# Performance work log

Measured on AMD Instinct MI355X. Metric: run time of the kernel, lower is better.

## Reference

```python
import jax, jax.numpy as jnp
import numpy as np

LENGTH = 512
Q = 2 * LENGTH + 3  # num_states = 2*length + 3
ALPHA = 26          # amino-acid alphabet size
BATCH = 256
T = 512


def setup_inputs() -> dict:
    key = jax.random.key(0)
    k1, k2, k3, k4 = jax.random.split(key, 4)
    x = jax.random.randint(k1, (BATCH, T), 0, ALPHA, dtype=jnp.int32)
    A_logits = jax.random.normal(k2, (Q, Q), dtype=jnp.float32)
    B_logits = jax.random.normal(k3, (Q, ALPHA), dtype=jnp.float32)
    init_logits = jax.random.normal(k4, (Q,), dtype=jnp.float32)
    return {"x": x, "A_logits": A_logits, "B_logits": B_logits, "init_logits": init_logits}


def reference(x, A_logits, B_logits, init_logits):
    # Build stochastic matrices (as emitter/transitioner do from their kernels).
    A = jax.nn.softmax(A_logits, axis=-1)        # (q, q) row-stochastic transitions
    B = jax.nn.softmax(B_logits, axis=-1)        # (q, alpha) emission distributions
    init = jax.nn.softmax(init_logits)           # (q,) initial distribution

    # Precompute per-position emission probs: E[b, t, :] = B[:, x[b, t]]
    E = B.T[x]                                   # (B, T, q)

    # First step (self.init branch): forward = E0 * initial distribution
    f0 = E[:, 0] * init[None, :]                 # (B, q)
    S0 = jnp.sum(f0, axis=-1, keepdims=True)     # (B, 1)
    ll0 = jnp.log(S0)
    f0 = f0 / S0

    def step(carry, Et):
        f, ll = carry
        fwd = Et * (f @ A)                       # emit * transition  (B, q)
        S = jnp.sum(fwd, axis=-1, keepdims=True)
        ll = ll + jnp.log(S)
        fwd = fwd / S
        return (fwd, ll), fwd

    (_, loglik), fwd_seq = jax.lax.scan(step, (f0, ll0), jnp.swapaxes(E[:, 1:], 0, 1))
    # fwd_seq: (T-1, B, q) -> full (B, T, q) with first step prepended
    forward = jnp.swapaxes(jnp.concatenate([f0[None], fwd_seq], axis=0), 0, 1)
    return forward, loglik
```

## Files before the change

kernel.cpp:

```cpp
#include <hip/hip_runtime.h>
#include <stdint.h>


#define Q     1027
#define TT    512
#define NBAT  256
#define ALPH  26
#define KH    1056
#define KCH   33
#define NTILE 65
#define ROWB  2128
#define GEXB  (16*ROWB)
#define NCL   16
#define WPC   16
#define MB    16

typedef short  short8  __attribute__((ext_vector_type(8)));
typedef float  floatx4 __attribute__((ext_vector_type(4)));
typedef int    intx4   __attribute__((ext_vector_type(4)));

static constexpr size_t al512(size_t x) { return (x + 511) & ~size_t(511); }
static constexpr size_t OFF_APACK = 0;
static constexpr size_t SZ_APACK  = (size_t)NTILE * KCH * 64 * 16;
static constexpr size_t OFF_BSOFT = al512(OFF_APACK + SZ_APACK);
static constexpr size_t SZ_BSOFT  = (size_t)Q * ALPH * 4;
static constexpr size_t OFF_INIT  = al512(OFF_BSOFT + SZ_BSOFT);
static constexpr size_t OFF_AMAX  = al512(OFF_INIT + Q * 4);
static constexpr size_t OFF_AINV  = al512(OFF_AMAX + Q * 4);
static constexpr size_t OFF_GEX   = al512(OFF_AINV + Q * 4);
static constexpr size_t SZ_GEX    = (size_t)NCL * 2 * GEXB + 1024;
static constexpr size_t OFF_FLAGS = al512(OFF_GEX + SZ_GEX);
static constexpr size_t SZ_FLAGS  = (size_t)NCL * WPC * 4;
static constexpr size_t OFF_SPART = al512(OFF_FLAGS + SZ_FLAGS);
static constexpr size_t SZ_SPART  = (size_t)NCL * 2 * WPC * MB * 4;
static constexpr size_t WS_NEED   = OFF_SPART + SZ_SPART;
static constexpr size_t FWDSZ     = (size_t)NBAT * TT * Q;

__device__ __forceinline__ uint32_t f2bf(float f) {
  uint32_t u = __float_as_uint(f);
  return (u + 0x7fffu + ((u >> 16) & 1u)) >> 16;
}


__global__ void k_zero(char* __restrict__ ws) {
  const size_t n = (WS_NEED - OFF_GEX) / 16;
  intx4* p = (intx4*)(ws + OFF_GEX);
  for (size_t i = (size_t)blockIdx.x * 256 + threadIdx.x; i < n; i += (size_t)275 * 256)
    p[i] = intx4{0, 0, 0, 0};
}

__global__ void k_astats(const float* __restrict__ A, char* __restrict__ ws) {
  const int r = blockIdx.x, tid = threadIdx.x;
  const float* row = A + (size_t)r * Q;
  __shared__ float red[4], red2[4];
  float mx = -3.0e38f;
  for (int i = tid; i < Q; i += 256) mx = fmaxf(mx, row[i]);
#pragma unroll
  for (int d = 1; d < 64; d <<= 1) mx = fmaxf(mx, __shfl_xor(mx, d));
  if ((tid & 63) == 0) red[tid >> 6] = mx;
  __syncthreads();
  mx = fmaxf(fmaxf(red[0], red[1]), fmaxf(red[2], red[3]));
  float s = 0.f;
  for (int i = tid; i < Q; i += 256) s += expf(row[i] - mx);
#pragma unroll
  for (int d = 1; d < 64; d <<= 1) s += __shfl_xor(s, d);
  if ((tid & 63) == 0) red2[tid >> 6] = s;
  __syncthreads();
  s = red2[0] + red2[1] + red2[2] + red2[3];
  if (tid == 0) {
    *(float*)(ws + OFF_AMAX + (size_t)r * 4) = mx;
    *(float*)(ws + OFF_AINV + (size_t)r * 4) = 1.0f / s;
  }
}

__global__ void k_bsoft(const float* __restrict__ Bl, char* __restrict__ ws) {
  const int r = blockIdx.x, l = threadIdx.x;
  float v = (l < ALPH) ? Bl[(size_t)r * ALPH + l] : -3.0e38f;
  float mx = v;
#pragma unroll
  for (int d = 1; d < 64; d <<= 1) mx = fmaxf(mx, __shfl_xor(mx, d));
  float e = (l < ALPH) ? expf(v - mx) : 0.f;
  float s = e;
#pragma unroll
  for (int d = 1; d < 64; d <<= 1) s += __shfl_xor(s, d);
  if (l < ALPH) *(float*)(ws + OFF_BSOFT + ((size_t)r * ALPH + l) * 4) = e / s;
}

__global__ void k_isoft(const float* __restrict__ il, char* __restrict__ ws) {
  const int tid = threadIdx.x;
  __shared__ float red[4], red2[4];
  float mx = -3.0e38f;
  for (int i = tid; i < Q; i += 256) mx = fmaxf(mx, il[i]);
#pragma unroll
  for (int d = 1; d < 64; d <<= 1) mx = fmaxf(mx, __shfl_xor(mx, d));
  if ((tid & 63) == 0) red[tid >> 6] = mx;
  __syncthreads();
  mx = fmaxf(fmaxf(red[0], red[1]), fmaxf(red[2], red[3]));
  float s = 0.f;
  for (int i = tid; i < Q; i += 256) s += expf(il[i] - mx);
#pragma unroll
  for (int d = 1; d < 64; d <<= 1) s += __shfl_xor(s, d);
  if ((tid & 63) == 0) red2[tid >> 6] = s;
  __syncthreads();
  s = red2[0] + red2[1] + red2[2] + red2[3];
  const float inv = 1.0f / s;
  for (int i = tid; i < Q; i += 256)
    *(float*)(ws + OFF_INIT + (size_t)i * 4) = expf(il[i] - mx) * inv;
}

__global__ void k_repack(const float* __restrict__ A, char* __restrict__ ws) {
  const int b = blockIdx.x;
  const int nt = b % NTILE, kc = b / NTILE;
  const int lane = threadIdx.x;
  const int q = nt * 16 + (lane & 15);
  const int kb = kc * 32 + (lane >> 4) * 8;
  union { short8 v; unsigned short u[8]; } pk;
#pragma unroll
  for (int e = 0; e < 8; ++e) {
    const int k = kb + e;
    float val = 0.f;
    if (k < Q && q < Q) {
      const float mxk = *(const float*)(ws + OFF_AMAX + (size_t)k * 4);
      const float ivk = *(const float*)(ws + OFF_AINV + (size_t)k * 4);
      val = expf(A[(size_t)k * Q + q] - mxk) * ivk;
    }
    pk.u[e] = (unsigned short)f2bf(val);
  }
  *(short8*)(ws + OFF_APACK + (((size_t)nt * KCH + kc) * 64 + lane) * 16) = pk.v;
}


__global__ __launch_bounds__(256) void k_main(const int* __restrict__ xin,
                                              char* __restrict__ ws,
                                              float* __restrict__ out) {
  const int bid = blockIdx.x;
  const int c = bid & 15, j = bid >> 4;
  const int tid = threadIdx.x;
  const int lane = tid & 63, w = tid >> 6;
  const int cL = lane & 15, g4 = lane >> 4;
  const bool j15 = (j == 15), two = (j15 && w == 3);
  const int t0 = 4 * j + w;
  const int col0 = t0 * 16;
  const int ntl = j15 ? 5 : 4;
  const uint64_t wsu = (uint64_t)(uintptr_t)ws;

  __shared__ intx4   g_lds4[2176 + 16];
  __shared__ uint8_t x_lds[MB * TT];
  __shared__ float   B_lds[5][16][ALPH];
  __shared__ float   init_lds[5][16];
  __shared__ float   Sp_lds[4][16];
  __shared__ float   accx_lds[4][64][4];

  for (int idx = tid; idx < MB * TT; idx += 256)
    x_lds[idx] = (uint8_t)xin[(size_t)(c * MB) * TT + idx];
  for (int idx = tid; idx < ntl * 16 * ALPH; idx += 256) {
    const int tl = idx / (16 * ALPH), rem = idx % (16 * ALPH);
    const int cc = rem / ALPH, a = rem % ALPH;
    const int grow = (tl < 4 ? 64 * j + tl * 16 : 1024) + cc;
    B_lds[tl][cc][a] = (grow < Q) ? *(const float*)(ws + OFF_BSOFT + ((size_t)grow * ALPH + a) * 4) : 0.f;
  }
  for (int idx = tid; idx < ntl * 16; idx += 256) {
    const int tl = idx / 16, cc = idx % 16;
    const int grow = (tl < 4 ? 64 * j + tl * 16 : 1024) + cc;
    init_lds[tl][cc] = (grow < Q) ? *(const float*)(ws + OFF_INIT + (size_t)grow * 4) : 0.f;
  }

  short8 af0[KCH];
#pragma unroll
  for (int kc = 0; kc < KCH; ++kc)
    af0[kc] = *(const short8*)(ws + OFF_APACK + (((size_t)t0 * KCH + kc) * 64 + lane) * 16);
  short8 af64[9];
  if (j15) {
#pragma unroll
    for (int i = 0; i < 9; ++i) {
      if (i < 8 || w == 3) {
        const int kc = w * 8 + i;
        af64[i] = *(const short8*)(ws + OFF_APACK + (((size_t)64 * KCH + kc) * 64 + lane) * 16);
      }
    }
  }
  __syncthreads();

  float up0[4], up1[4] = {0.f, 0.f, 0.f, 0.f};

#pragma unroll
  for (int r = 0; r < 4; ++r) {
    const int m = g4 * 4 + r;
    const int xm = x_lds[m * TT + 0];
    up0[r] = B_lds[w][cL][xm] * init_lds[w][cL];
    if (two) up1[r] = B_lds[4][cL][xm] * init_lds[4][cL];
  }

#define POST_STEP(TCUR)                                                                   \
  do {                                                                                    \
    const int par_ = (TCUR) & 1;                                                          \
    const uint64_t gb_ = wsu + OFF_GEX + (size_t)(c * 2 + par_) * GEXB;                   \
    float tmp_[4];                                                                        \
    _Pragma("unroll") for (int r = 0; r < 4; ++r) {                                       \
      const int m_ = g4 * 4 + r;                                                          \
      uint32_t b0_ = f2bf(up0[r]);                                                        \
      asm volatile("global_store_short %0, %1, off sc0 sc1" ::                            \
                   "v"(gb_ + (size_t)m_ * ROWB + (size_t)(col0 + cL) * 2), "v"(b0_)       \
                   : "memory");                                                           \
      tmp_[r] = up0[r];                                                                   \
      if (two) {                                                                          \
        uint32_t b1_ = f2bf(up1[r]);                                                      \
        asm volatile("global_store_short %0, %1, off sc0 sc1" ::                          \
                     "v"(gb_ + (size_t)m_ * ROWB + (size_t)(1024 + cL) * 2), "v"(b1_)     \
                     : "memory");                                                         \
        tmp_[r] += up1[r];                                                                \
      }                                                                                   \
    }                                                                                     \
    _Pragma("unroll") for (int r = 0; r < 4; ++r) {                                       \
      _Pragma("unroll") for (int d = 1; d < 16; d <<= 1) tmp_[r] += __shfl_xor(tmp_[r], d); \
    }                                                                                     \
    if (cL == 0) {                                                                        \
      _Pragma("unroll") for (int r = 0; r < 4; ++r) Sp_lds[w][g4 * 4 + r] = tmp_[r];      \
    }                                                                                     \
    asm volatile("s_waitcnt vmcnt(0)" ::: "memory");                                      \
    __syncthreads();                                                                      \
    if (w == 0) {                                                                         \
      if (lane < 16) {                                                                    \
        float sw_ = Sp_lds[0][lane] + Sp_lds[1][lane] + Sp_lds[2][lane] + Sp_lds[3][lane];\
        uint64_t sa_ = wsu + OFF_SPART + (size_t)(((c * 2 + par_) * WPC + j) * MB + lane) * 4; \
        asm volatile("global_store_dword %0, %1, off sc0 sc1\n\ts_waitcnt vmcnt(0)" ::    \
                     "v"(sa_), "v"(sw_) : "memory");                                      \
      }                                                                                   \
      if (lane == 0) {                                                                    \
        uint64_t fa_ = wsu + OFF_FLAGS + (size_t)(c * WPC + j) * 4;                       \
        int fv_ = (TCUR) + 1;                                                             \
        asm volatile("global_store_dword %0, %1, off sc0 sc1" :: "v"(fa_), "v"(fv_)       \
                     : "memory");                                                         \
      }                                                                                   \
    }                                                                                     \
  } while (0)

#define WAIT_FLAGS(TGT)                                                                   \
  do {                                                                                    \
    if (w == 0) {                                                                         \
      const uint64_t fa_ = wsu + OFF_FLAGS + (size_t)(c * WPC + cL) * 4;                  \
      for (;;) {                                                                          \
        int f_;                                                                           \
        asm volatile("global_load_dword %0, %1, off sc0 sc1\n\ts_waitcnt vmcnt(0)"        \
                     : "=v"(f_) : "v"(fa_) : "memory");                                   \
        if (__all(f_ >= (TGT))) break;                                                    \
        __builtin_amdgcn_s_sleep(2);                                                      \
      }                                                                                   \
    }                                                                                     \
    __syncthreads();                                                                      \
  } while (0)

#define SPART_BLOCK(PARP, SVAR)                                                           \
  float SVAR;                                                                             \
  do {                                                                                    \
    const uint64_t sb_ = wsu + OFF_SPART + (size_t)((c * 2 + (PARP)) * WPC) * MB * 4;     \
    float p0_, p1_, p2_, p3_;                                                             \
    uint64_t a0_ = sb_ + (size_t)((g4 + 0) * MB + cL) * 4;                                \
    uint64_t a1_ = sb_ + (size_t)((g4 + 4) * MB + cL) * 4;                                \
    uint64_t a2_ = sb_ + (size_t)((g4 + 8) * MB + cL) * 4;                                \
    uint64_t a3_ = sb_ + (size_t)((g4 + 12) * MB + cL) * 4;                               \
    asm volatile("global_load_dword %0, %4, off sc0 sc1\n\t"                              \
                 "global_load_dword %1, %5, off sc0 sc1\n\t"                              \
                 "global_load_dword %2, %6, off sc0 sc1\n\t"                              \
                 "global_load_dword %3, %7, off sc0 sc1\n\t"                              \
                 "s_waitcnt vmcnt(0)"                                                     \
                 : "=v"(p0_), "=v"(p1_), "=v"(p2_), "=v"(p3_)                             \
                 : "v"(a0_), "v"(a1_), "v"(a2_), "v"(a3_) : "memory");                    \
    SVAR = p0_ + p1_ + p2_ + p3_;                                                         \
    SVAR += __shfl_xor(SVAR, 16);                                                         \
    SVAR += __shfl_xor(SVAR, 32);                                                         \
  } while (0)

  POST_STEP(0);

  float llacc = 0.f;

  for (int t = 1; t < TT; ++t) {
    const int parp = (t - 1) & 1;

    WAIT_FLAGS(t);

    const uint64_t gbp = wsu + OFF_GEX + (size_t)(c * 2 + parp) * GEXB;
    intx4 sgv[9];
#pragma unroll
    for (int i = 0; i < 8; ++i) {
      uint64_t a = gbp + (size_t)((i * 256 + tid) * 16);
      asm volatile("global_load_dwordx4 %0, %1, off sc0 sc1" : "=v"(sgv[i]) : "v"(a) : "memory");
    }
    const bool has9 = (tid < 80);
    if (has9) {
      uint64_t a = gbp + (size_t)((2048 + tid) * 16);
      asm volatile("global_load_dwordx4 %0, %1, off sc0 sc1" : "=v"(sgv[8]) : "v"(a) : "memory");
    }

    SPART_BLOCK(parp, s);

#pragma unroll
    for (int i = 0; i < 8; ++i) g_lds4[i * 256 + tid] = sgv[i];
    if (has9) g_lds4[2048 + tid] = sgv[8];

    if (j == 0 && w == 0) llacc += logf(s);
    float invS[4];
#pragma unroll
    for (int r = 0; r < 4; ++r) invS[r] = 1.0f / __shfl(s, g4 * 4 + r);

#pragma unroll
    for (int r = 0; r < 4; ++r) {
      const int m = g4 * 4 + r;
      const size_t ob = ((size_t)(c * MB + m) * TT + (t - 1)) * Q;
      __builtin_nontemporal_store(up0[r] * invS[r], out + ob + col0 + cL);
      if (two && cL < 3)
        __builtin_nontemporal_store(up1[r] * invS[r], out + ob + 1024 + cL);
    }
    __syncthreads();

    floatx4 a0v = {0, 0, 0, 0}, a1v = {0, 0, 0, 0}, a64v = {0, 0, 0, 0};
    const char* gl = (const char*)g_lds4;
    const int gof = cL * ROWB + g4 * 16;
#pragma unroll
    for (int kc = 0; kc < KCH; ++kc) {
      short8 gf = *(const short8*)(gl + gof + kc * 64);
      if (kc & 1) a1v = __builtin_amdgcn_mfma_f32_16x16x32_bf16(gf, af0[kc], a1v, 0, 0, 0);
      else        a0v = __builtin_amdgcn_mfma_f32_16x16x32_bf16(gf, af0[kc], a0v, 0, 0, 0);
    }
    float r1v[4];
    if (j15) {
#pragma unroll
      for (int i = 0; i < 9; ++i) {
        if (i < 8 || w == 3) {
          const int kc = w * 8 + i;
          short8 gf = *(const short8*)(gl + gof + kc * 64);
          a64v = __builtin_amdgcn_mfma_f32_16x16x32_bf16(gf, af64[i], a64v, 0, 0, 0);
        }
      }
#pragma unroll
      for (int r = 0; r < 4; ++r) accx_lds[w][lane][r] = a64v[r];
      __syncthreads();
      if (two) {
#pragma unroll
        for (int r = 0; r < 4; ++r)
          r1v[r] = accx_lds[0][lane][r] + accx_lds[1][lane][r] +
                   accx_lds[2][lane][r] + accx_lds[3][lane][r];
      }
    }

#pragma unroll
    for (int r = 0; r < 4; ++r) {
      const int m = g4 * 4 + r;
      const int xm = x_lds[m * TT + t];
      up0[r] = (a0v[r] + a1v[r]) * B_lds[w][cL][xm] * invS[r];
      if (two) up1[r] = r1v[r] * B_lds[4][cL][xm] * invS[r];
    }

    POST_STEP(t);
  }

  WAIT_FLAGS(TT);
  {
    SPART_BLOCK((TT - 1) & 1, s);
    if (j == 0 && w == 0) llacc += logf(s);
    float invS[4];
#pragma unroll
    for (int r = 0; r < 4; ++r) invS[r] = 1.0f / __shfl(s, g4 * 4 + r);
#pragma unroll
    for (int r = 0; r < 4; ++r) {
      const int m = g4 * 4 + r;
      const size_t ob = ((size_t)(c * MB + m) * TT + (TT - 1)) * Q;
      __builtin_nontemporal_store(up0[r] * invS[r], out + ob + col0 + cL);
      if (two && cL < 3)
        __builtin_nontemporal_store(up1[r] * invS[r], out + ob + 1024 + cL);
    }
    if (j == 0 && w == 0 && lane < 16) out[FWDSZ + (size_t)c * MB + lane] = llacc;
  }
}


extern "C" void kernel_launch(void* const* d_in, const int* in_sizes, int n_in,
                              void* d_out, int out_size, void* d_ws, size_t ws_size,
                              hipStream_t stream) {
  const int*   x    = (const int*)d_in[0];
  const float* Alog = (const float*)d_in[1];
  const float* Blog = (const float*)d_in[2];
  const float* ilog = (const float*)d_in[3];
  char*  ws  = (char*)d_ws;
  float* out = (float*)d_out;
  if (ws_size < WS_NEED) return;

  hipLaunchKernelGGL(k_zero,   dim3(275),         dim3(256), 0, stream, ws);
  hipLaunchKernelGGL(k_astats, dim3(Q),           dim3(256), 0, stream, Alog, ws);
  hipLaunchKernelGGL(k_bsoft,  dim3(Q),           dim3(64),  0, stream, Blog, ws);
  hipLaunchKernelGGL(k_isoft,  dim3(1),           dim3(256), 0, stream, ilog, ws);
  hipLaunchKernelGGL(k_repack, dim3(NTILE * KCH), dim3(64),  0, stream, Alog, ws);
  hipLaunchKernelGGL(k_main,   dim3(256),         dim3(256), 0, stream, x, ws, out);
}
```

Before: 2.418 ms.

## Restructure HMM forward kernel to 512-thread blocks with per-wave flags and pre-packed MFMA exchange

Moves from 256 blocks of 4 waves to 128 blocks of 8 waves, so each cluster of batch rows spans 8 workgroups instead of 16. Every wave publishes its own flag and partial sums, which removes the intra-block barrier before signalling. The exchange buffer is written directly in MFMA fragment layout so it can be loaded with wide coalesced loads. The MFMA loop is split so the first half of the K chunks runs while the second half of the exchange buffer is still loading. It adds 64-lane flag polling and more LDS use per block, and relies on a correct cross-workgroup memory ordering with the new layout.

```diff
diff --git a/kernel.cpp b/kernel.cpp
--- a/kernel.cpp
+++ b/kernel.cpp
@@ -4,15 +4,12 @@
 
 #define Q     1027
 #define TT    512
-#define NBAT  256
 #define ALPH  26
-#define KH    1056
 #define KCH   33
 #define NTILE 65
-#define ROWB  2128
-#define GEXB  (16*ROWB)
+#define GIMG  (KCH*64*16)
 #define NCL   16
-#define WPC   16
+#define WPC   8
 #define MB    16
 
 typedef short  short8  __attribute__((ext_vector_type(8)));
@@ -28,13 +25,13 @@
 static constexpr size_t OFF_AMAX  = al512(OFF_INIT + Q * 4);
 static constexpr size_t OFF_AINV  = al512(OFF_AMAX + Q * 4);
 static constexpr size_t OFF_GEX   = al512(OFF_AINV + Q * 4);
-static constexpr size_t SZ_GEX    = (size_t)NCL * 2 * GEXB + 1024;
-static constexpr size_t OFF_FLAGS = al512(OFF_GEX + SZ_GEX);
-static constexpr size_t SZ_FLAGS  = (size_t)NCL * WPC * 4;
-static constexpr size_t OFF_SPART = al512(OFF_FLAGS + SZ_FLAGS);
-static constexpr size_t SZ_SPART  = (size_t)NCL * 2 * WPC * MB * 4;
-static constexpr size_t WS_NEED   = OFF_SPART + SZ_SPART;
-static constexpr size_t FWDSZ     = (size_t)NBAT * TT * Q;
+static constexpr size_t SZ_GEX    = (size_t)NCL * 2 * GIMG;
+static constexpr size_t OFF_SP    = al512(OFF_GEX + SZ_GEX);
+static constexpr size_t SZ_SP     = (size_t)NCL * 2 * 64 * MB * 4;
+static constexpr size_t OFF_FLAGS = al512(OFF_SP + SZ_SP);
+static constexpr size_t SZ_FLAGS  = (size_t)NCL * 64 * 4;
+static constexpr size_t WS_NEED   = OFF_FLAGS + SZ_FLAGS;
+static constexpr size_t FWDSZ     = (size_t)256 * TT * Q;
 
 __device__ __forceinline__ uint32_t f2bf(float f) {
   uint32_t u = __float_as_uint(f);
@@ -43,10 +40,8 @@
 
 
 __global__ void k_zero(char* __restrict__ ws) {
-  const size_t n = (WS_NEED - OFF_GEX) / 16;
-  intx4* p = (intx4*)(ws + OFF_GEX);
-  for (size_t i = (size_t)blockIdx.x * 256 + threadIdx.x; i < n; i += (size_t)275 * 256)
-    p[i] = intx4{0, 0, 0, 0};
+  const int i = blockIdx.x * 256 + threadIdx.x;
+  if (i < (int)(SZ_FLAGS / 4)) ((int*)(ws + OFF_FLAGS))[i] = 0;
 }
 
 __global__ void k_astats(const float* __restrict__ A, char* __restrict__ ws) {
@@ -130,7 +125,7 @@
 }
 
 
-__global__ __launch_bounds__(256) void k_main(const int* __restrict__ xin,
+__global__ __launch_bounds__(512) void k_main(const int* __restrict__ xin,
                                               char* __restrict__ ws,
                                               float* __restrict__ out) {
   const int bid = blockIdx.x;
@@ -138,209 +133,222 @@
   const int tid = threadIdx.x;
   const int lane = tid & 63, w = tid >> 6;
   const int cL = lane & 15, g4 = lane >> 4;
-  const bool j15 = (j == 15), two = (j15 && w == 3);
-  const int t0 = 4 * j + w;
-  const int col0 = t0 * 16;
-  const int ntl = j15 ? 5 : 4;
+  const int tg = 8 * j + w;
+  const int col0 = tg * 16;
+  const bool jx = (j == 7);
+  const bool own64 = (jx && w == 7);
+  const int kc0x = 4 * w;
+  const int ncx = (w == 7) ? 5 : 4;
   const uint64_t wsu = (uint64_t)(uintptr_t)ws;
 
-  __shared__ intx4   g_lds4[2176 + 16];
+  __shared__ intx4   g_lds[2112];
+  __shared__ float   B_lds[9][16][ALPH];
   __shared__ uint8_t x_lds[MB * TT];
-  __shared__ float   B_lds[5][16][ALPH];
-  __shared__ float   init_lds[5][16];
-  __shared__ float   Sp_lds[4][16];
-  __shared__ float   accx_lds[4][64][4];
-
-  for (int idx = tid; idx < MB * TT; idx += 256)
+  __shared__ floatx4 accx[7][64];
+  __shared__ float   init_lds[9][16];
+  __shared__ float   SpL[2][16];
+
+  for (int idx = tid; idx < MB * TT; idx += 512)
     x_lds[idx] = (uint8_t)xin[(size_t)(c * MB) * TT + idx];
-  for (int idx = tid; idx < ntl * 16 * ALPH; idx += 256) {
+  for (int idx = tid; idx < 9 * 16 * ALPH; idx += 512) {
     const int tl = idx / (16 * ALPH), rem = idx % (16 * ALPH);
     const int cc = rem / ALPH, a = rem % ALPH;
-    const int grow = (tl < 4 ? 64 * j + tl * 16 : 1024) + cc;
+    const int grow = (tl < 8 ? 16 * (8 * j + tl) : 1024) + cc;
     B_lds[tl][cc][a] = (grow < Q) ? *(const float*)(ws + OFF_BSOFT + ((size_t)grow * ALPH + a) * 4) : 0.f;
   }
-  for (int idx = tid; idx < ntl * 16; idx += 256) {
-    const int tl = idx / 16, cc = idx % 16;
-    const int grow = (tl < 4 ? 64 * j + tl * 16 : 1024) + cc;
+  for (int idx = tid; idx < 9 * 16; idx += 512) {
+    const int tl = idx >> 4, cc = idx & 15;
+    const int grow = (tl < 8 ? 16 * (8 * j + tl) : 1024) + cc;
     init_lds[tl][cc] = (grow < Q) ? *(const float*)(ws + OFF_INIT + (size_t)grow * 4) : 0.f;
   }
 
   short8 af0[KCH];
 #pragma unroll
   for (int kc = 0; kc < KCH; ++kc)
-    af0[kc] = *(const short8*)(ws + OFF_APACK + (((size_t)t0 * KCH + kc) * 64 + lane) * 16);
-  short8 af64[9];
-  if (j15) {
-#pragma unroll
-    for (int i = 0; i < 9; ++i) {
-      if (i < 8 || w == 3) {
-        const int kc = w * 8 + i;
-        af64[i] = *(const short8*)(ws + OFF_APACK + (((size_t)64 * KCH + kc) * 64 + lane) * 16);
-      }
+    af0[kc] = *(const short8*)(ws + OFF_APACK + (((size_t)tg * KCH + kc) * 64 + lane) * 16);
+  short8 afx[5];
+  if (jx) {
+#pragma unroll
+    for (int i = 0; i < 5; ++i) {
+      if (i < ncx)
+        afx[i] = *(const short8*)(ws + OFF_APACK + (((size_t)64 * KCH + kc0x + i) * 64 + lane) * 16);
     }
   }
   __syncthreads();
 
-  float up0[4], up1[4] = {0.f, 0.f, 0.f, 0.f};
+  float upc[4], upx[4] = {0.f, 0.f, 0.f, 0.f};
+  float llacc = 0.f;
+
+#define POSTSTEP(TCUR)                                                                    \
+  do {                                                                                    \
+    const int par_ = (TCUR) & 1;                                                          \
+    const uint64_t gb_ = wsu + OFF_GEX + (size_t)(c * 2 + par_) * GIMG;                   \
+    const uint64_t spb_ = wsu + OFF_SP + (size_t)(c * 2 + par_) * 4096;                   \
+    const int sub_ = (2 * tg + (cL >> 3)) & 3;                                            \
+    const uint64_t ga_ = gb_ + (size_t)((tg >> 1) * 1024) + (size_t)(16 * sub_) * 16 +    \
+                         (size_t)(cL & 7) * 2;                                            \
+    float tmp0_ = upc[0], tmp1_ = upc[1], tmp2_ = upc[2], tmp3_ = upc[3];                 \
+    _Pragma("unroll") for (int r = 0; r < 4; ++r) {                                       \
+      const int m_ = g4 * 4 + r;                                                          \
+      uint32_t b_ = f2bf(upc[r]);                                                         \
+      asm volatile("global_store_short %0, %1, off sc0 sc1" ::                            \
+                   "v"(ga_ + (size_t)m_ * 16), "v"(b_) : "memory");                       \
+    }                                                                                     \
+    if (own64) {                                                                          \
+      const uint64_t gx_ = gb_ + (size_t)(32 * 1024) + (size_t)((cL >> 3) * 16) * 16 +    \
+                           (size_t)(cL & 7) * 2;                                          \
+      _Pragma("unroll") for (int r = 0; r < 4; ++r) {                                     \
+        const int m_ = g4 * 4 + r;                                                        \
+        uint32_t b_ = f2bf(upx[r]);                                                       \
+        asm volatile("global_store_short %0, %1, off sc0 sc1" ::                          \
+                     "v"(gx_ + (size_t)m_ * 16), "v"(b_) : "memory");                     \
+      }                                                                                   \
+      tmp0_ += upx[0]; tmp1_ += upx[1]; tmp2_ += upx[2]; tmp3_ += upx[3];                 \
+    }                                                                                     \
+    _Pragma("unroll") for (int d_ = 1; d_ < 16; d_ <<= 1) {                               \
+      tmp0_ += __shfl_xor(tmp0_, d_); tmp1_ += __shfl_xor(tmp1_, d_);                     \
+      tmp2_ += __shfl_xor(tmp2_, d_); tmp3_ += __shfl_xor(tmp3_, d_);                     \
+    }                                                                                     \
+    if (cL == 0) {                                                                        \
+      uint64_t sa_ = spb_ + (size_t)((8 * j + w) * 16 + g4 * 4) * 4;                      \
+      asm volatile("global_store_dword %0, %1, off sc0 sc1" :: "v"(sa_), "v"(tmp0_) : "memory");     \
+      asm volatile("global_store_dword %0, %1, off sc0 sc1" :: "v"(sa_ + 4), "v"(tmp1_) : "memory"); \
+      asm volatile("global_store_dword %0, %1, off sc0 sc1" :: "v"(sa_ + 8), "v"(tmp2_) : "memory"); \
+      asm volatile("global_store_dword %0, %1, off sc0 sc1" :: "v"(sa_ + 12), "v"(tmp3_) : "memory");\
+    }                                                                                     \
+    asm volatile("s_waitcnt vmcnt(0)" ::: "memory");                                      \
+    __builtin_amdgcn_sched_barrier(0);                                                    \
+    if (lane == 0) {                                                                      \
+      uint64_t fa_ = wsu + OFF_FLAGS + (size_t)(c * 64 + 8 * j + w) * 4;                  \
+      int fv_ = (TCUR) + 1;                                                               \
+      asm volatile("global_store_dword %0, %1, off sc0 sc1" :: "v"(fa_), "v"(fv_) : "memory"); \
+    }                                                                                     \
+  } while (0)
+
+#define WAITF(TGT)                                                                        \
+  do {                                                                                    \
+    const uint64_t fa_ = wsu + OFF_FLAGS + (size_t)(c * 64 + lane) * 4;                   \
+    for (;;) {                                                                            \
+      int f_;                                                                             \
+      asm volatile("global_load_dword %0, %1, off sc0 sc1\n\ts_waitcnt vmcnt(0)"          \
+                   : "=v"(f_) : "v"(fa_) : "memory");                                     \
+      if (__all(f_ >= (TGT))) break;                                                      \
+      __builtin_amdgcn_s_sleep(1);                                                        \
+    }                                                                                     \
+  } while (0)
 
 #pragma unroll
   for (int r = 0; r < 4; ++r) {
     const int m = g4 * 4 + r;
     const int xm = x_lds[m * TT + 0];
-    up0[r] = B_lds[w][cL][xm] * init_lds[w][cL];
-    if (two) up1[r] = B_lds[4][cL][xm] * init_lds[4][cL];
-  }
-
-#define POST_STEP(TCUR)                                                                   \
-  do {                                                                                    \
-    const int par_ = (TCUR) & 1;                                                          \
-    const uint64_t gb_ = wsu + OFF_GEX + (size_t)(c * 2 + par_) * GEXB;                   \
-    float tmp_[4];                                                                        \
-    _Pragma("unroll") for (int r = 0; r < 4; ++r) {                                       \
-      const int m_ = g4 * 4 + r;                                                          \
-      uint32_t b0_ = f2bf(up0[r]);                                                        \
-      asm volatile("global_store_short %0, %1, off sc0 sc1" ::                            \
-                   "v"(gb_ + (size_t)m_ * ROWB + (size_t)(col0 + cL) * 2), "v"(b0_)       \
-                   : "memory");                                                           \
-      tmp_[r] = up0[r];                                                                   \
-      if (two) {                                                                          \
-        uint32_t b1_ = f2bf(up1[r]);                                                      \
-        asm volatile("global_store_short %0, %1, off sc0 sc1" ::                          \
-                     "v"(gb_ + (size_t)m_ * ROWB + (size_t)(1024 + cL) * 2), "v"(b1_)     \
-                     : "memory");                                                         \
-        tmp_[r] += up1[r];                                                                \
-      }                                                                                   \
-    }                                                                                     \
-    _Pragma("unroll") for (int r = 0; r < 4; ++r) {                                       \
-      _Pragma("unroll") for (int d = 1; d < 16; d <<= 1) tmp_[r] += __shfl_xor(tmp_[r], d); \
-    }                                                                                     \
-    if (cL == 0) {                                                                        \
-      _Pragma("unroll") for (int r = 0; r < 4; ++r) Sp_lds[w][g4 * 4 + r] = tmp_[r];      \
-    }                                                                                     \
-    asm volatile("s_waitcnt vmcnt(0)" ::: "memory");                                      \
-    __syncthreads();                                                                      \
-    if (w == 0) {                                                                         \
-      if (lane < 16) {                                                                    \
-        float sw_ = Sp_lds[0][lane] + Sp_lds[1][lane] + Sp_lds[2][lane] + Sp_lds[3][lane];\
-        uint64_t sa_ = wsu + OFF_SPART + (size_t)(((c * 2 + par_) * WPC + j) * MB + lane) * 4; \
-        asm volatile("global_store_dword %0, %1, off sc0 sc1\n\ts_waitcnt vmcnt(0)" ::    \
-                     "v"(sa_), "v"(sw_) : "memory");                                      \
-      }                                                                                   \
-      if (lane == 0) {                                                                    \
-        uint64_t fa_ = wsu + OFF_FLAGS + (size_t)(c * WPC + j) * 4;                       \
-        int fv_ = (TCUR) + 1;                                                             \
-        asm volatile("global_store_dword %0, %1, off sc0 sc1" :: "v"(fa_), "v"(fv_)       \
-                     : "memory");                                                         \
-      }                                                                                   \
-    }                                                                                     \
-  } while (0)
-
-#define WAIT_FLAGS(TGT)                                                                   \
-  do {                                                                                    \
-    if (w == 0) {                                                                         \
-      const uint64_t fa_ = wsu + OFF_FLAGS + (size_t)(c * WPC + cL) * 4;                  \
-      for (;;) {                                                                          \
-        int f_;                                                                           \
-        asm volatile("global_load_dword %0, %1, off sc0 sc1\n\ts_waitcnt vmcnt(0)"        \
-                     : "=v"(f_) : "v"(fa_) : "memory");                                   \
-        if (__all(f_ >= (TGT))) break;                                                    \
-        __builtin_amdgcn_s_sleep(2);                                                      \
-      }                                                                                   \
-    }                                                                                     \
-    __syncthreads();                                                                      \
-  } while (0)
-
-#define SPART_BLOCK(PARP, SVAR)                                                           \
-  float SVAR;                                                                             \
-  do {                                                                                    \
-    const uint64_t sb_ = wsu + OFF_SPART + (size_t)((c * 2 + (PARP)) * WPC) * MB * 4;     \
-    float p0_, p1_, p2_, p3_;                                                             \
-    uint64_t a0_ = sb_ + (size_t)((g4 + 0) * MB + cL) * 4;                                \
-    uint64_t a1_ = sb_ + (size_t)((g4 + 4) * MB + cL) * 4;                                \
-    uint64_t a2_ = sb_ + (size_t)((g4 + 8) * MB + cL) * 4;                                \
-    uint64_t a3_ = sb_ + (size_t)((g4 + 12) * MB + cL) * 4;                               \
-    asm volatile("global_load_dword %0, %4, off sc0 sc1\n\t"                              \
-                 "global_load_dword %1, %5, off sc0 sc1\n\t"                              \
-                 "global_load_dword %2, %6, off sc0 sc1\n\t"                              \
-                 "global_load_dword %3, %7, off sc0 sc1\n\t"                              \
-                 "s_waitcnt vmcnt(0)"                                                     \
-                 : "=v"(p0_), "=v"(p1_), "=v"(p2_), "=v"(p3_)                             \
-                 : "v"(a0_), "v"(a1_), "v"(a2_), "v"(a3_) : "memory");                    \
-    SVAR = p0_ + p1_ + p2_ + p3_;                                                         \
-    SVAR += __shfl_xor(SVAR, 16);                                                         \
-    SVAR += __shfl_xor(SVAR, 32);                                                         \
-  } while (0)
-
-  POST_STEP(0);
-
-  float llacc = 0.f;
+    upc[r] = B_lds[w][cL][xm] * init_lds[w][cL];
+    if (own64) upx[r] = B_lds[8][cL][xm] * init_lds[8][cL];
+  }
+  POSTSTEP(0);
 
   for (int t = 1; t < TT; ++t) {
     const int parp = (t - 1) & 1;
-
-    WAIT_FLAGS(t);
-
-    const uint64_t gbp = wsu + OFF_GEX + (size_t)(c * 2 + parp) * GEXB;
-    intx4 sgv[9];
-#pragma unroll
-    for (int i = 0; i < 8; ++i) {
-      uint64_t a = gbp + (size_t)((i * 256 + tid) * 16);
-      asm volatile("global_load_dwordx4 %0, %1, off sc0 sc1" : "=v"(sgv[i]) : "v"(a) : "memory");
-    }
-    const bool has9 = (tid < 80);
-    if (has9) {
-      uint64_t a = gbp + (size_t)((2048 + tid) * 16);
-      asm volatile("global_load_dwordx4 %0, %1, off sc0 sc1" : "=v"(sgv[8]) : "v"(a) : "memory");
-    }
-
-    SPART_BLOCK(parp, s);
-
-#pragma unroll
-    for (int i = 0; i < 8; ++i) g_lds4[i * 256 + tid] = sgv[i];
-    if (has9) g_lds4[2048 + tid] = sgv[8];
-
-    if (j == 0 && w == 0) llacc += logf(s);
+    WAITF(t);
+
+    const uint64_t gb = wsu + OFF_GEX + (size_t)(c * 2 + parp) * GIMG;
+    const uint64_t spb = wsu + OFF_SP + (size_t)(c * 2 + parp) * 4096;
+    floatx4 sp0 = {0, 0, 0, 0}, sp1 = {0, 0, 0, 0};
+    intx4 r0, r1, r2, r3, tl4;
+    if (tid < 128) {
+      uint64_t sa = spb + (size_t)tid * 32;
+      asm volatile("global_load_dwordx4 %0, %1, off sc0 sc1" : "=v"(sp0) : "v"(sa) : "memory");
+      asm volatile("global_load_dwordx4 %0, %1, off sc0 sc1" : "=v"(sp1) : "v"(sa + 16) : "memory");
+    }
+    if (tid < 64) {
+      asm volatile("global_load_dwordx4 %0, %1, off sc0 sc1"
+                   : "=v"(tl4) : "v"(gb + (size_t)(2048 + tid) * 16) : "memory");
+    }
+    asm volatile("global_load_dwordx4 %0, %1, off sc0 sc1" : "=v"(r0) : "v"(gb + (size_t)tid * 16) : "memory");
+    asm volatile("global_load_dwordx4 %0, %1, off sc0 sc1" : "=v"(r1) : "v"(gb + (size_t)(512 + tid) * 16) : "memory");
+    asm volatile("global_load_dwordx4 %0, %1, off sc0 sc1" : "=v"(r2) : "v"(gb + (size_t)(1024 + tid) * 16) : "memory");
+    asm volatile("global_load_dwordx4 %0, %1, off sc0 sc1" : "=v"(r3) : "v"(gb + (size_t)(1536 + tid) * 16) : "memory");
+    asm volatile("s_waitcnt vmcnt(2)" ::: "memory");
+    __builtin_amdgcn_sched_barrier(0);
+    g_lds[tid] = r0;
+    g_lds[512 + tid] = r1;
+    if (tid < 128) {
+#pragma unroll
+      for (int d = 2; d < 64; d <<= 1) {
+#pragma unroll
+        for (int e = 0; e < 4; ++e) { sp0[e] += __shfl_xor(sp0[e], d); sp1[e] += __shfl_xor(sp1[e], d); }
+      }
+      if (lane < 2) {
+        const int mb = (lane & 1) * 8;
+#pragma unroll
+        for (int e = 0; e < 4; ++e) { SpL[w][mb + e] = sp0[e]; SpL[w][mb + 4 + e] = sp1[e]; }
+      }
+    }
+    __syncthreads();
+
+    floatx4 a0v = {0, 0, 0, 0}, a1v = {0, 0, 0, 0}, axv = {0, 0, 0, 0};
+    const char* gl = (const char*)g_lds;
+#pragma unroll
+    for (int kc = 0; kc < 16; ++kc) {
+      short8 gf = *(const short8*)(gl + (kc * 64 + lane) * 16);
+      if (kc & 1) a1v = __builtin_amdgcn_mfma_f32_16x16x32_bf16(gf, af0[kc], a1v, 0, 0, 0);
+      else        a0v = __builtin_amdgcn_mfma_f32_16x16x32_bf16(gf, af0[kc], a0v, 0, 0, 0);
+    }
+    if (jx && kc0x < 16) {
+#pragma unroll
+      for (int i = 0; i < 4; ++i) {
+        short8 gf = *(const short8*)(gl + ((kc0x + i) * 64 + lane) * 16);
+        axv = __builtin_amdgcn_mfma_f32_16x16x32_bf16(gf, afx[i], axv, 0, 0, 0);
+      }
+    }
+    asm volatile("s_waitcnt vmcnt(0)" ::: "memory");
+    __builtin_amdgcn_sched_barrier(0);
+    g_lds[1024 + tid] = r2;
+    g_lds[1536 + tid] = r3;
+    if (tid < 64) g_lds[2048 + tid] = tl4;
+    __syncthreads();
+
     float invS[4];
 #pragma unroll
-    for (int r = 0; r < 4; ++r) invS[r] = 1.0f / __shfl(s, g4 * 4 + r);
-
+    for (int r = 0; r < 4; ++r) {
+      const int m = g4 * 4 + r;
+      invS[r] = 1.0f / (SpL[0][m] + SpL[1][m]);
+    }
+    if (j == 0 && w == 0 && lane < 16) llacc += logf(SpL[0][lane] + SpL[1][lane]);
 #pragma unroll
     for (int r = 0; r < 4; ++r) {
       const int m = g4 * 4 + r;
       const size_t ob = ((size_t)(c * MB + m) * TT + (t - 1)) * Q;
-      __builtin_nontemporal_store(up0[r] * invS[r], out + ob + col0 + cL);
-      if (two && cL < 3)
-        __builtin_nontemporal_store(up1[r] * invS[r], out + ob + 1024 + cL);
-    }
-    __syncthreads();
-
-    floatx4 a0v = {0, 0, 0, 0}, a1v = {0, 0, 0, 0}, a64v = {0, 0, 0, 0};
-    const char* gl = (const char*)g_lds4;
-    const int gof = cL * ROWB + g4 * 16;
-#pragma unroll
-    for (int kc = 0; kc < KCH; ++kc) {
-      short8 gf = *(const short8*)(gl + gof + kc * 64);
+      __builtin_nontemporal_store(upc[r] * invS[r], out + ob + col0 + cL);
+      if (own64 && cL < 3)
+        __builtin_nontemporal_store(upx[r] * invS[r], out + ob + 1024 + cL);
+    }
+
+#pragma unroll
+    for (int kc = 16; kc < KCH; ++kc) {
+      short8 gf = *(const short8*)(gl + (kc * 64 + lane) * 16);
       if (kc & 1) a1v = __builtin_amdgcn_mfma_f32_16x16x32_bf16(gf, af0[kc], a1v, 0, 0, 0);
       else        a0v = __builtin_amdgcn_mfma_f32_16x16x32_bf16(gf, af0[kc], a0v, 0, 0, 0);
     }
-    float r1v[4];
-    if (j15) {
-#pragma unroll
-      for (int i = 0; i < 9; ++i) {
-        if (i < 8 || w == 3) {
-          const int kc = w * 8 + i;
-          short8 gf = *(const short8*)(gl + gof + kc * 64);
-          a64v = __builtin_amdgcn_mfma_f32_16x16x32_bf16(gf, af64[i], a64v, 0, 0, 0);
+    if (jx && kc0x >= 16) {
+#pragma unroll
+      for (int i = 0; i < 5; ++i) {
+        if (i < ncx) {
+          short8 gf = *(const short8*)(gl + ((kc0x + i) * 64 + lane) * 16);
+          axv = __builtin_amdgcn_mfma_f32_16x16x32_bf16(gf, afx[i], axv, 0, 0, 0);
         }
       }
-#pragma unroll
-      for (int r = 0; r < 4; ++r) accx_lds[w][lane][r] = a64v[r];
+    }
+    float rx[4] = {0.f, 0.f, 0.f, 0.f};
+    if (jx) {
+      if (w < 7) accx[w][lane] = axv;
       __syncthreads();
-      if (two) {
-#pragma unroll
-        for (int r = 0; r < 4; ++r)
-          r1v[r] = accx_lds[0][lane][r] + accx_lds[1][lane][r] +
-                   accx_lds[2][lane][r] + accx_lds[3][lane][r];
+      if (own64) {
+#pragma unroll
+        for (int r = 0; r < 4; ++r) {
+          rx[r] = axv[r];
+#pragma unroll
+          for (int i = 0; i < 7; ++i) rx[r] += accx[i][lane][r];
+        }
       }
     }
 
@@ -348,27 +356,49 @@
     for (int r = 0; r < 4; ++r) {
       const int m = g4 * 4 + r;
       const int xm = x_lds[m * TT + t];
-      up0[r] = (a0v[r] + a1v[r]) * B_lds[w][cL][xm] * invS[r];
-      if (two) up1[r] = r1v[r] * B_lds[4][cL][xm] * invS[r];
-    }
-
-    POST_STEP(t);
-  }
-
-  WAIT_FLAGS(TT);
+      upc[r] = (a0v[r] + a1v[r]) * B_lds[w][cL][xm] * invS[r];
+      if (own64) upx[r] = rx[r] * B_lds[8][cL][xm] * invS[r];
+    }
+    POSTSTEP(t);
+  }
+
+  WAITF(TT);
   {
-    SPART_BLOCK((TT - 1) & 1, s);
-    if (j == 0 && w == 0) llacc += logf(s);
+    const int parp = (TT - 1) & 1;
+    const uint64_t spb = wsu + OFF_SP + (size_t)(c * 2 + parp) * 4096;
+    floatx4 sp0 = {0, 0, 0, 0}, sp1 = {0, 0, 0, 0};
+    if (tid < 128) {
+      uint64_t sa = spb + (size_t)tid * 32;
+      asm volatile("global_load_dwordx4 %0, %1, off sc0 sc1" : "=v"(sp0) : "v"(sa) : "memory");
+      asm volatile("global_load_dwordx4 %0, %1, off sc0 sc1" : "=v"(sp1) : "v"(sa + 16) : "memory");
+      asm volatile("s_waitcnt vmcnt(0)" ::: "memory");
+      __builtin_amdgcn_sched_barrier(0);
+#pragma unroll
+      for (int d = 2; d < 64; d <<= 1) {
+#pragma unroll
+        for (int e = 0; e < 4; ++e) { sp0[e] += __shfl_xor(sp0[e], d); sp1[e] += __shfl_xor(sp1[e], d); }
+      }
+      if (lane < 2) {
+        const int mb = (lane & 1) * 8;
+#pragma unroll
+        for (int e = 0; e < 4; ++e) { SpL[w][mb + e] = sp0[e]; SpL[w][mb + 4 + e] = sp1[e]; }
+      }
+    }
+    __syncthreads();
     float invS[4];
 #pragma unroll
-    for (int r = 0; r < 4; ++r) invS[r] = 1.0f / __shfl(s, g4 * 4 + r);
+    for (int r = 0; r < 4; ++r) {
+      const int m = g4 * 4 + r;
+      invS[r] = 1.0f / (SpL[0][m] + SpL[1][m]);
+    }
+    if (j == 0 && w == 0 && lane < 16) llacc += logf(SpL[0][lane] + SpL[1][lane]);
 #pragma unroll
     for (int r = 0; r < 4; ++r) {
       const int m = g4 * 4 + r;
       const size_t ob = ((size_t)(c * MB + m) * TT + (TT - 1)) * Q;
-      __builtin_nontemporal_store(up0[r] * invS[r], out + ob + col0 + cL);
-      if (two && cL < 3)
-        __builtin_nontemporal_store(up1[r] * invS[r], out + ob + 1024 + cL);
+      __builtin_nontemporal_store(upc[r] * invS[r], out + ob + col0 + cL);
+      if (own64 && cL < 3)
+        __builtin_nontemporal_store(upx[r] * invS[r], out + ob + 1024 + cL);
     }
     if (j == 0 && w == 0 && lane < 16) out[FWDSZ + (size_t)c * MB + lane] = llacc;
   }
@@ -386,10 +416,10 @@
   float* out = (float*)d_out;
   if (ws_size < WS_NEED) return;
 
-  hipLaunchKernelGGL(k_zero,   dim3(275),         dim3(256), 0, stream, ws);
+  hipLaunchKernelGGL(k_zero,   dim3(4),           dim3(256), 0, stream, ws);
   hipLaunchKernelGGL(k_astats, dim3(Q),           dim3(256), 0, stream, Alog, ws);
   hipLaunchKernelGGL(k_bsoft,  dim3(Q),           dim3(64),  0, stream, Blog, ws);
   hipLaunchKernelGGL(k_isoft,  dim3(1),           dim3(256), 0, stream, ilog, ws);
   hipLaunchKernelGGL(k_repack, dim3(NTILE * KCH), dim3(64),  0, stream, Alog, ws);
-  hipLaunchKernelGGL(k_main,   dim3(256),         dim3(256), 0, stream, x, ws, out);
-}
+  hipLaunchKernelGGL(k_main,   dim3(128),         dim3(512), 0, stream, x, ws, out);
+}
```

After: 5.332 ms. 2.21x slower.

## Store exchanged forward vector in MFMA fragment order to drop padded row layout

Applied to the files above, without the earlier changes.

The bf16 forward-state exchange buffer moves from a padded row-major layout (16 rows of ROWB bytes) to a layout already arranged as MFMA A-operand fragments. Each wave then reads its operands with a contiguous per-lane LDS load, without strided row offsets, and the exchange image shrinks. The global stores in the post-step now scatter shorts into fragment positions, and the log-likelihood accumulation is moved after the post-step so it is off the critical path before publishing. It also shrinks the zeroing grid and makes B/init loading uniform.

```diff
diff --git a/kernel.cpp b/kernel.cpp
--- a/kernel.cpp
+++ b/kernel.cpp
@@ -4,13 +4,11 @@
 
 #define Q     1027
 #define TT    512
-#define NBAT  256
 #define ALPH  26
-#define KH    1056
 #define KCH   33
 #define NTILE 65
-#define ROWB  2128
-#define GEXB  (16*ROWB)
+#define NCHK  (KCH*64)
+#define GIMG  (NCHK*16)
 #define NCL   16
 #define WPC   16
 #define MB    16
@@ -28,13 +26,13 @@
 static constexpr size_t OFF_AMAX  = al512(OFF_INIT + Q * 4);
 static constexpr size_t OFF_AINV  = al512(OFF_AMAX + Q * 4);
 static constexpr size_t OFF_GEX   = al512(OFF_AINV + Q * 4);
-static constexpr size_t SZ_GEX    = (size_t)NCL * 2 * GEXB + 1024;
+static constexpr size_t SZ_GEX    = (size_t)NCL * 2 * GIMG;
 static constexpr size_t OFF_FLAGS = al512(OFF_GEX + SZ_GEX);
 static constexpr size_t SZ_FLAGS  = (size_t)NCL * WPC * 4;
 static constexpr size_t OFF_SPART = al512(OFF_FLAGS + SZ_FLAGS);
 static constexpr size_t SZ_SPART  = (size_t)NCL * 2 * WPC * MB * 4;
 static constexpr size_t WS_NEED   = OFF_SPART + SZ_SPART;
-static constexpr size_t FWDSZ     = (size_t)NBAT * TT * Q;
+static constexpr size_t FWDSZ     = (size_t)256 * TT * Q;
 
 __device__ __forceinline__ uint32_t f2bf(float f) {
   uint32_t u = __float_as_uint(f);
@@ -45,7 +43,7 @@
 __global__ void k_zero(char* __restrict__ ws) {
   const size_t n = (WS_NEED - OFF_GEX) / 16;
   intx4* p = (intx4*)(ws + OFF_GEX);
-  for (size_t i = (size_t)blockIdx.x * 256 + threadIdx.x; i < n; i += (size_t)275 * 256)
+  for (size_t i = (size_t)blockIdx.x * 256 + threadIdx.x; i < n; i += (size_t)72 * 256)
     p[i] = intx4{0, 0, 0, 0};
 }
 
@@ -138,13 +136,11 @@
   const int tid = threadIdx.x;
   const int lane = tid & 63, w = tid >> 6;
   const int cL = lane & 15, g4 = lane >> 4;
-  const bool j15 = (j == 15), two = (j15 && w == 3);
-  const int t0 = 4 * j + w;
-  const int col0 = t0 * 16;
-  const int ntl = j15 ? 5 : 4;
+  const bool jx = (j == 15), two = (jx && w == 3);
+  const int tg = 4 * j + w;
   const uint64_t wsu = (uint64_t)(uintptr_t)ws;
 
-  __shared__ intx4   g_lds4[2176 + 16];
+  __shared__ intx4   g_lds[NCHK];
   __shared__ uint8_t x_lds[MB * TT];
   __shared__ float   B_lds[5][16][ALPH];
   __shared__ float   init_lds[5][16];
@@ -153,13 +149,13 @@
 
   for (int idx = tid; idx < MB * TT; idx += 256)
     x_lds[idx] = (uint8_t)xin[(size_t)(c * MB) * TT + idx];
-  for (int idx = tid; idx < ntl * 16 * ALPH; idx += 256) {
+  for (int idx = tid; idx < 5 * 16 * ALPH; idx += 256) {
     const int tl = idx / (16 * ALPH), rem = idx % (16 * ALPH);
     const int cc = rem / ALPH, a = rem % ALPH;
     const int grow = (tl < 4 ? 64 * j + tl * 16 : 1024) + cc;
     B_lds[tl][cc][a] = (grow < Q) ? *(const float*)(ws + OFF_BSOFT + ((size_t)grow * ALPH + a) * 4) : 0.f;
   }
-  for (int idx = tid; idx < ntl * 16; idx += 256) {
+  for (int idx = tid; idx < 5 * 16; idx += 256) {
     const int tl = idx / 16, cc = idx % 16;
     const int grow = (tl < 4 ? 64 * j + tl * 16 : 1024) + cc;
     init_lds[tl][cc] = (grow < Q) ? *(const float*)(ws + OFF_INIT + (size_t)grow * 4) : 0.f;
@@ -168,9 +164,9 @@
   short8 af0[KCH];
 #pragma unroll
   for (int kc = 0; kc < KCH; ++kc)
-    af0[kc] = *(const short8*)(ws + OFF_APACK + (((size_t)t0 * KCH + kc) * 64 + lane) * 16);
+    af0[kc] = *(const short8*)(ws + OFF_APACK + (((size_t)tg * KCH + kc) * 64 + lane) * 16);
   short8 af64[9];
-  if (j15) {
+  if (jx) {
 #pragma unroll
     for (int i = 0; i < 9; ++i) {
       if (i < 8 || w == 3) {
@@ -183,31 +179,24 @@
 
   float up0[4], up1[4] = {0.f, 0.f, 0.f, 0.f};
 
-#pragma unroll
-  for (int r = 0; r < 4; ++r) {
-    const int m = g4 * 4 + r;
-    const int xm = x_lds[m * TT + 0];
-    up0[r] = B_lds[w][cL][xm] * init_lds[w][cL];
-    if (two) up1[r] = B_lds[4][cL][xm] * init_lds[4][cL];
-  }
-
 #define POST_STEP(TCUR)                                                                   \
   do {                                                                                    \
     const int par_ = (TCUR) & 1;                                                          \
-    const uint64_t gb_ = wsu + OFF_GEX + (size_t)(c * 2 + par_) * GEXB;                   \
+    const uint64_t gb_ = wsu + OFF_GEX + (size_t)(c * 2 + par_) * GIMG;                   \
+    const uint64_t b0_ = gb_ + (size_t)((tg >> 1) * 1024 + ((tg & 1) * 2 + (cL >> 3)) * 256 \
+                         + g4 * 64 + (cL & 7) * 2);                                       \
     float tmp_[4];                                                                        \
     _Pragma("unroll") for (int r = 0; r < 4; ++r) {                                       \
-      const int m_ = g4 * 4 + r;                                                          \
-      uint32_t b0_ = f2bf(up0[r]);                                                        \
+      uint32_t v0_ = f2bf(up0[r]);                                                        \
       asm volatile("global_store_short %0, %1, off sc0 sc1" ::                            \
-                   "v"(gb_ + (size_t)m_ * ROWB + (size_t)(col0 + cL) * 2), "v"(b0_)       \
-                   : "memory");                                                           \
+                   "v"(b0_ + (size_t)(r * 16)), "v"(v0_) : "memory");                     \
       tmp_[r] = up0[r];                                                                   \
       if (two) {                                                                          \
-        uint32_t b1_ = f2bf(up1[r]);                                                      \
+        const uint64_t bx_ = gb_ + (size_t)(32 * 1024 + (cL >> 3) * 256 + g4 * 64 +       \
+                             (cL & 7) * 2);                                               \
+        uint32_t v1_ = f2bf(up1[r]);                                                      \
         asm volatile("global_store_short %0, %1, off sc0 sc1" ::                          \
-                     "v"(gb_ + (size_t)m_ * ROWB + (size_t)(1024 + cL) * 2), "v"(b1_)     \
-                     : "memory");                                                         \
+                     "v"(bx_ + (size_t)(r * 16)), "v"(v1_) : "memory");                   \
         tmp_[r] += up1[r];                                                                \
       }                                                                                   \
     }                                                                                     \
@@ -271,6 +260,13 @@
     SVAR += __shfl_xor(SVAR, 32);                                                         \
   } while (0)
 
+#pragma unroll
+  for (int r = 0; r < 4; ++r) {
+    const int m = g4 * 4 + r;
+    const int xm = x_lds[m * TT + 0];
+    up0[r] = B_lds[w][cL][xm] * init_lds[w][cL];
+    if (two) up1[r] = B_lds[4][cL][xm] * init_lds[4][cL];
+  }
   POST_STEP(0);
 
   float llacc = 0.f;
@@ -280,26 +276,25 @@
 
     WAIT_FLAGS(t);
 
-    const uint64_t gbp = wsu + OFF_GEX + (size_t)(c * 2 + parp) * GEXB;
-    intx4 sgv[9];
+    const uint64_t gbp = wsu + OFF_GEX + (size_t)(c * 2 + parp) * GIMG;
+    intx4 sgv[8], tl4;
 #pragma unroll
     for (int i = 0; i < 8; ++i) {
       uint64_t a = gbp + (size_t)((i * 256 + tid) * 16);
       asm volatile("global_load_dwordx4 %0, %1, off sc0 sc1" : "=v"(sgv[i]) : "v"(a) : "memory");
     }
-    const bool has9 = (tid < 80);
+    const bool has9 = (tid < 64);
     if (has9) {
       uint64_t a = gbp + (size_t)((2048 + tid) * 16);
-      asm volatile("global_load_dwordx4 %0, %1, off sc0 sc1" : "=v"(sgv[8]) : "v"(a) : "memory");
+      asm volatile("global_load_dwordx4 %0, %1, off sc0 sc1" : "=v"(tl4) : "v"(a) : "memory");
     }
 
     SPART_BLOCK(parp, s);
 
 #pragma unroll
-    for (int i = 0; i < 8; ++i) g_lds4[i * 256 + tid] = sgv[i];
-    if (has9) g_lds4[2048 + tid] = sgv[8];
-
-    if (j == 0 && w == 0) llacc += logf(s);
+    for (int i = 0; i < 8; ++i) g_lds[i * 256 + tid] = sgv[i];
+    if (has9) g_lds[2048 + tid] = tl4;
+
     float invS[4];
 #pragma unroll
     for (int r = 0; r < 4; ++r) invS[r] = 1.0f / __shfl(s, g4 * 4 + r);
@@ -308,28 +303,26 @@
     for (int r = 0; r < 4; ++r) {
       const int m = g4 * 4 + r;
       const size_t ob = ((size_t)(c * MB + m) * TT + (t - 1)) * Q;
-      __builtin_nontemporal_store(up0[r] * invS[r], out + ob + col0 + cL);
+      __builtin_nontemporal_store(up0[r] * invS[r], out + ob + tg * 16 + cL);
       if (two && cL < 3)
         __builtin_nontemporal_store(up1[r] * invS[r], out + ob + 1024 + cL);
     }
     __syncthreads();
 
     floatx4 a0v = {0, 0, 0, 0}, a1v = {0, 0, 0, 0}, a64v = {0, 0, 0, 0};
-    const char* gl = (const char*)g_lds4;
-    const int gof = cL * ROWB + g4 * 16;
 #pragma unroll
     for (int kc = 0; kc < KCH; ++kc) {
-      short8 gf = *(const short8*)(gl + gof + kc * 64);
+      short8 gf = *(const short8*)&g_lds[kc * 64 + lane];
       if (kc & 1) a1v = __builtin_amdgcn_mfma_f32_16x16x32_bf16(gf, af0[kc], a1v, 0, 0, 0);
       else        a0v = __builtin_amdgcn_mfma_f32_16x16x32_bf16(gf, af0[kc], a0v, 0, 0, 0);
     }
     float r1v[4];
-    if (j15) {
+    if (jx) {
 #pragma unroll
       for (int i = 0; i < 9; ++i) {
         if (i < 8 || w == 3) {
           const int kc = w * 8 + i;
-          short8 gf = *(const short8*)(gl + gof + kc * 64);
+          short8 gf = *(const short8*)&g_lds[kc * 64 + lane];
           a64v = __builtin_amdgcn_mfma_f32_16x16x32_bf16(gf, af64[i], a64v, 0, 0, 0);
         }
       }
@@ -353,6 +346,7 @@
     }
 
     POST_STEP(t);
+    if (j == 0 && w == 0) llacc += logf(s);
   }
 
   WAIT_FLAGS(TT);
@@ -366,7 +360,7 @@
     for (int r = 0; r < 4; ++r) {
       const int m = g4 * 4 + r;
       const size_t ob = ((size_t)(c * MB + m) * TT + (TT - 1)) * Q;
-      __builtin_nontemporal_store(up0[r] * invS[r], out + ob + col0 + cL);
+      __builtin_nontemporal_store(up0[r] * invS[r], out + ob + tg * 16 + cL);
       if (two && cL < 3)
         __builtin_nontemporal_store(up1[r] * invS[r], out + ob + 1024 + cL);
     }
@@ -386,10 +380,10 @@
   float* out = (float*)d_out;
   if (ws_size < WS_NEED) return;
 
-  hipLaunchKernelGGL(k_zero,   dim3(275),         dim3(256), 0, stream, ws);
+  hipLaunchKernelGGL(k_zero,   dim3(72),          dim3(256), 0, stream, ws);
   hipLaunchKernelGGL(k_astats, dim3(Q),           dim3(256), 0, stream, Alog, ws);
   hipLaunchKernelGGL(k_bsoft,  dim3(Q),           dim3(64),  0, stream, Blog, ws);
   hipLaunchKernelGGL(k_isoft,  dim3(1),           dim3(256), 0, stream, ilog, ws);
   hipLaunchKernelGGL(k_repack, dim3(NTILE * KCH), dim3(64),  0, stream, Alog, ws);
-  hipLaunchKernelGGL(k_main,   dim3(256),         dim3(256), 0, stream, x, ws, out);
-}
+  hipLaunchKernelGGL(k_main,   dim3(NCL * WPC),   dim3(256), 0, stream, x, ws, out);
+}
```

New measurement: 2.258 ms. 1.07x faster.
